# Performance work log

Measured on AMD Instinct MI355X. Metric: run time of the kernel, lower is better.

## Reference

```python
import jax, jax.numpy as jnp
import numpy as np
import math

DIM = 1024
N_HEADS = 16
HEAD_DIM = DIM // N_HEADS
FFN_HIDDEN = 4096
EPS = 1e-6


def setup_inputs() -> dict:
    key = jax.random.key(0)
    ks = jax.random.split(key, 10)
    s = 1.0 / math.sqrt(DIM)
    sh = 1.0 / math.sqrt(FFN_HIDDEN)
    return {
        "x": jax.random.normal(ks[0], (2, 2048, DIM), dtype=jnp.float32),
        # attention weights stored as [in, out] (y = x @ W)
        "wq": jax.random.normal(ks[1], (DIM, DIM), dtype=jnp.float32) * s,
        "wk": jax.random.normal(ks[2], (DIM, DIM), dtype=jnp.float32) * s,
        "wv": jax.random.normal(ks[3], (DIM, DIM), dtype=jnp.float32) * s,
        "wo": jax.random.normal(ks[4], (DIM, DIM), dtype=jnp.float32) * s,
        "w_gate": jax.random.normal(ks[5], (DIM, FFN_HIDDEN), dtype=jnp.float32) * s,
        "w_up": jax.random.normal(ks[6], (DIM, FFN_HIDDEN), dtype=jnp.float32) * s,
        "w_down": jax.random.normal(ks[7], (FFN_HIDDEN, DIM), dtype=jnp.float32) * sh,
        "attn_norm_w": jnp.ones((DIM,), dtype=jnp.float32),
        "ffn_norm_w": jnp.ones((DIM,), dtype=jnp.float32),
    }


def rmsnorm(x, w):
    xf = x.astype(jnp.float32)
    rms = jax.lax.rsqrt(jnp.mean(xf * xf, axis=-1, keepdims=True) + EPS)
    return (xf * rms).astype(x.dtype) * w


def attention(x, wq, wk, wv, wo):
    B, T, C = x.shape
    q = (x @ wq).reshape(B, T, N_HEADS, HEAD_DIM)
    k = (x @ wk).reshape(B, T, N_HEADS, HEAD_DIM)
    v = (x @ wv).reshape(B, T, N_HEADS, HEAD_DIM)
    scores = jnp.einsum("bqhd,bkhd->bhqk", q, k) / math.sqrt(HEAD_DIM)
    causal = jnp.tril(jnp.ones((T, T), dtype=bool))  # True = keep
    scores = jnp.where(causal, scores, -jnp.inf)
    attn = jax.nn.softmax(scores, axis=-1)
    out = jnp.einsum("bhqk,bkhd->bqhd", attn, v).reshape(B, T, C)
    return out @ wo


def swiglu(x, w_gate, w_up, w_down):
    return (jax.nn.silu(x @ w_gate) * (x @ w_up)) @ w_down


def reference(x, wq, wk, wv, wo, w_gate, w_up, w_down, attn_norm_w, ffn_norm_w):
    x = x + attention(rmsnorm(x, attn_norm_w), wq, wk, wv, wo)
    x = x + swiglu(rmsnorm(x, ffn_norm_w), w_gate, w_up, w_down)
    return x
```

## Files before the change

kernel.cpp:

```cpp
#include <hip/hip_runtime.h>
#include <hip/hip_bf16.h>
#include <stdint.h>
#include <math.h>

#define DIM   1024
#define TSEQ  2048
#define BATCH 2
#define NH    16
#define HD    64
#define FFN   4096
#define ROWS  (BATCH*TSEQ)
#define QKVN  (3*DIM)

typedef __attribute__((ext_vector_type(8))) short s16x8;
typedef __attribute__((ext_vector_type(4))) float f32x4;

__device__ __forceinline__ unsigned short f2bf(float f) {
  union { float f; unsigned u; } v; v.f = f;
  unsigned r = v.u + 0x7fffu + ((v.u >> 16) & 1u);
  return (unsigned short)(r >> 16);
}
__device__ __forceinline__ float bf2f(unsigned short h) {
  union { unsigned u; float f; } v; v.u = ((unsigned)h) << 16; return v.f;
}
__device__ __forceinline__ unsigned pack_bf2(float lo, float hi) {
  union { float f; unsigned u; } a, c; a.f = lo; c.f = hi;
  return (c.u & 0xffff0000u) | (a.u >> 16);
}

__device__ __forceinline__ void gld16(const void* g, void* l) {
  __builtin_amdgcn_global_load_lds((const __attribute__((address_space(1))) void*)g,
                                   (__attribute__((address_space(3))) void*)l, 16, 0, 0);
}

__device__ __forceinline__ int xcd_swz_flat() {
  const int nx = gridDim.x, ny = gridDim.y;
  const int nwg = nx * ny * gridDim.z;
  const int flat = blockIdx.x + nx * (blockIdx.y + ny * blockIdx.z);
  return (flat & 7) * (nwg >> 3) + (flat >> 3);
}

__global__ void wtrans_k(const float* __restrict__ w, unsigned short* __restrict__ wt,
                         int K, int N, int mode)
{
  __shared__ unsigned short t[64][65];
  const int n0 = blockIdx.x * 64, k0 = blockIdx.y * 64;
  const int tid = threadIdx.x;
  #pragma unroll
  for (int i = 0; i < 16; ++i) {
    const int r = i*4 + (tid >> 6), c = tid & 63;
    t[r][c] = f2bf(w[(size_t)(k0 + r) * N + n0 + c]);
  }
  __syncthreads();
  #pragma unroll
  for (int i = 0; i < 16; ++i) {
    const int r = i*4 + (tid >> 6), c = tid & 63;
    const int n = n0 + r;
    int dr = n;
    if (mode == 1) dr = ((n >> 4) << 5) + (n & 15);
    if (mode == 2) dr = ((n >> 4) << 5) + 16 + (n & 15);
    wt[(size_t)dr * K + k0 + c] = t[c][r];
  }
}

__global__ void wtrans_qkv_k(const float* __restrict__ wq, const float* __restrict__ wk,
                             const float* __restrict__ wv, unsigned short* __restrict__ wt)
{
  __shared__ unsigned short t[64][65];
  const int n0 = blockIdx.x * 64, k0 = blockIdx.y * 64, z = blockIdx.z;
  const float* w = (z == 0) ? wq : (z == 1) ? wk : wv;
  unsigned short* dst = wt + (size_t)z * DIM * DIM;
  const int tid = threadIdx.x;
  #pragma unroll
  for (int i = 0; i < 16; ++i) {
    const int r = i*4 + (tid >> 6), c = tid & 63;
    t[r][c] = f2bf(w[(size_t)(k0 + r) * DIM + n0 + c]);
  }
  __syncthreads();
  #pragma unroll
  for (int i = 0; i < 16; ++i) {
    const int r = i*4 + (tid >> 6), c = tid & 63;
    dst[(size_t)(n0 + r) * DIM + k0 + c] = t[c][r];
  }
}

__global__ void vtrans_k(const unsigned short* __restrict__ qkv, unsigned short* __restrict__ vt)
{
  __shared__ unsigned short t[64][65];
  const int tt0 = blockIdx.x * 64;
  const int bh = blockIdx.y, b = bh >> 4, h = bh & 15;
  const int tid = threadIdx.x;
  const unsigned short* src = qkv + (size_t)(b*TSEQ + tt0) * QKVN + 2*DIM + h*HD;
  #pragma unroll
  for (int i = 0; i < 16; ++i) {
    const int r = i*4 + (tid >> 6), c = tid & 63;
    t[r][c] = src[(size_t)r * QKVN + c];
  }
  __syncthreads();
  unsigned short* dst = vt + (size_t)bh * HD * TSEQ + tt0;
  #pragma unroll
  for (int i = 0; i < 16; ++i) {
    const int d = i*4 + (tid >> 6), c = tid & 63;
    dst[(size_t)d * TSEQ + c] = t[c][d];
  }
}

__global__ void rmsnorm_k(const float* __restrict__ x, const float* __restrict__ w,
                          unsigned short* __restrict__ o)
{
  const int row = blockIdx.x, tid = threadIdx.x;
  const float4 v = ((const float4*)(x + (size_t)row * DIM))[tid];
  float ss = v.x*v.x + v.y*v.y + v.z*v.z + v.w*v.w;
  #pragma unroll
  for (int off = 32; off >= 1; off >>= 1) ss += __shfl_xor(ss, off);
  __shared__ float sred[4];
  if ((tid & 63) == 0) sred[tid >> 6] = ss;
  __syncthreads();
  const float tot = sred[0] + sred[1] + sred[2] + sred[3];
  const float r = rsqrtf(tot * (1.0f/DIM) + 1e-6f);
  const float4 wv = ((const float4*)w)[tid];
  ushort4 ov;
  ov.x = f2bf(v.x*r*wv.x); ov.y = f2bf(v.y*r*wv.y);
  ov.z = f2bf(v.z*r*wv.z); ov.w = f2bf(v.w*r*wv.w);
  ((ushort4*)(o + (size_t)row * DIM))[tid] = ov;
}

__global__ void rmsnorm3_k(const float* __restrict__ x, const unsigned short* __restrict__ p0,
                           const unsigned short* __restrict__ p1, const float* __restrict__ w,
                           float* __restrict__ x1, unsigned short* __restrict__ o)
{
  const int row = blockIdx.x, tid = threadIdx.x;
  const size_t base = (size_t)row * DIM;
  const float4 a = ((const float4*)(x + base))[tid];
  const ushort4 b = ((const ushort4*)(p0 + base))[tid];
  const ushort4 c = ((const ushort4*)(p1 + base))[tid];
  float4 v;
  v.x = a.x + bf2f(b.x) + bf2f(c.x); v.y = a.y + bf2f(b.y) + bf2f(c.y);
  v.z = a.z + bf2f(b.z) + bf2f(c.z); v.w = a.w + bf2f(b.w) + bf2f(c.w);
  ((float4*)(x1 + base))[tid] = v;
  float ss = v.x*v.x + v.y*v.y + v.z*v.z + v.w*v.w;
  #pragma unroll
  for (int off = 32; off >= 1; off >>= 1) ss += __shfl_xor(ss, off);
  __shared__ float sred[4];
  if ((tid & 63) == 0) sred[tid >> 6] = ss;
  __syncthreads();
  const float tot = sred[0] + sred[1] + sred[2] + sred[3];
  const float r = rsqrtf(tot * (1.0f/DIM) + 1e-6f);
  const float4 wv = ((const float4*)w)[tid];
  ushort4 ov;
  ov.x = f2bf(v.x*r*wv.x); ov.y = f2bf(v.y*r*wv.y);
  ov.z = f2bf(v.z*r*wv.z); ov.w = f2bf(v.w*r*wv.w);
  ((ushort4*)(o + base))[tid] = ov;
}

__global__ void resadd5_k(const float* __restrict__ x1,
                          const unsigned short* __restrict__ q0, const unsigned short* __restrict__ q1,
                          const unsigned short* __restrict__ q2, const unsigned short* __restrict__ q3,
                          float* __restrict__ o)
{
  const size_t i = (size_t)blockIdx.x * 256 + threadIdx.x;
  const float4 a = ((const float4*)x1)[i];
  const ushort4 b = ((const ushort4*)q0)[i];
  const ushort4 c = ((const ushort4*)q1)[i];
  const ushort4 d = ((const ushort4*)q2)[i];
  const ushort4 e = ((const ushort4*)q3)[i];
  float4 v;
  v.x = a.x + bf2f(b.x) + bf2f(c.x) + bf2f(d.x) + bf2f(e.x);
  v.y = a.y + bf2f(b.y) + bf2f(c.y) + bf2f(d.y) + bf2f(e.y);
  v.z = a.z + bf2f(b.z) + bf2f(c.z) + bf2f(d.z) + bf2f(e.z);
  v.w = a.w + bf2f(b.w) + bf2f(c.w) + bf2f(d.w) + bf2f(e.w);
  ((float4*)o)[i] = v;
}

template<int NS>
__global__ void gemm128sp(const unsigned short* __restrict__ A, int lda,
                          const unsigned short* __restrict__ BT, int ldb,
                          unsigned short* __restrict__ P, int ldc, int Ksp)
{
  __shared__ __align__(16) unsigned short lA[128*64];
  __shared__ __align__(16) unsigned short lB[128*64];
  const int nx = gridDim.x, ny = gridDim.y;
  const int w = xcd_swz_flat();
  const int bx = w % nx, by = (w / nx) % ny, bz = w / (nx * ny);
  const int tid = threadIdx.x;
  const int lane = tid & 63;
  const int wid = tid >> 6;
  const int m0 = by * 128, n0 = bx * 128;
  const int Koff = bz * Ksp;
  P += (size_t)bz * ((size_t)ny * 128) * ldc;
  const int wr = (wid >> 1) * 64, wc = (wid & 1) * 64;
  const int lrow = lane & 15, lk8 = (lane >> 4) * 8;

  f32x4 acc[4][4] = {};

  for (int k0 = Koff; k0 < Koff + Ksp; k0 += 64) {
    #pragma unroll
    for (int c = 0; c < 4; ++c) {
      const int boff = c*4096 + tid*16;
      const int row = boff >> 7, colb = boff & 127;
      gld16((const char*)A + ((size_t)(m0+row)*lda + k0)*2 + colb, (char*)lA + boff);
    }
    #pragma unroll
    for (int c = 0; c < 4; ++c) {
      const int boff = c*4096 + tid*16;
      const int row = boff >> 7, colb = boff & 127;
      gld16((const char*)BT + ((size_t)(n0+row)*ldb + k0)*2 + colb, (char*)lB + boff);
    }
    __syncthreads();
    #pragma unroll
    for (int kk = 0; kk < 64; kk += 32) {
      s16x8 af[4], bf[4];
      #pragma unroll
      for (int i = 0; i < 4; ++i) af[i] = *(const s16x8*)&lA[(wr + i*16 + lrow)*64 + kk + lk8];
      #pragma unroll
      for (int j = 0; j < 4; ++j) bf[j] = *(const s16x8*)&lB[(wc + j*16 + lrow)*64 + kk + lk8];
      #pragma unroll
      for (int i = 0; i < 4; ++i)
        #pragma unroll
        for (int j = 0; j < 4; ++j)
          acc[i][j] = __builtin_amdgcn_mfma_f32_16x16x32_bf16(af[i], bf[j], acc[i][j], 0, 0, 0);
    }
    __syncthreads();
  }
  const int er = (lane >> 4) * 4, ec = lane & 15;
  #pragma unroll
  for (int i = 0; i < 4; ++i)
    #pragma unroll
    for (int j = 0; j < 4; ++j) {
      const int gr = m0 + wr + i*16 + er;
      const int gc = n0 + wc + j*16 + ec;
      #pragma unroll
      for (int e = 0; e < 4; ++e)
        P[(size_t)(gr + e) * ldc + gc] = f2bf(acc[i][j][e]);
    }
}

template<int EPI>
__global__ __launch_bounds__(512) void gemm256(const unsigned short* __restrict__ A, int lda,
                                               const unsigned short* __restrict__ BT, int ldb,
                                               void* __restrict__ Cout, int ldc, int K,
                                               int CX, int CY)
{
  __shared__ __align__(16) unsigned short lA[2][256*64];
  __shared__ __align__(16) unsigned short lB[2][256*64];
  const int nx = gridDim.x, ny = gridDim.y;
  const int flat = blockIdx.x + nx * blockIdx.y;
  const int xcd = flat & 7, k = flat >> 3;
  const int RX = nx / CX, RY = ny / CY;
  const int cx = xcd % CX, cy = xcd / CX;
  const int bx = cx * RX + k % RX;
  const int by = cy * RY + k / RX;
  const int tid = threadIdx.x, lane = tid & 63, wid = tid >> 6;
  const int lrow = lane & 15, g = lane >> 4;
  const int wm = wid >> 2, wn = wid & 3;
  const int m0 = by * 256, n0 = bx * 256;

  const int r0 = tid >> 3;
  const int eB = ((r0 >> 5) << 6) | (r0 & 31);
  const int lc0 = ((tid & 7) * 16) ^ ((r0 & 7) << 4);
  const char* pA = (const char*)A + ((size_t)(m0 + r0) * lda) * 2 + lc0;
  const char* pB = (const char*)BT + ((size_t)(n0 + eB) * ldb) * 2 + lc0;
  char* dA = (char*)&lA[0][0] + tid * 16;
  char* dB = (char*)&lB[0][0] + eB * 128 + (tid & 7) * 16;
  const size_t a64 = (size_t)64 * lda * 2;
  const size_t b32 = (size_t)32 * ldb * 2;

#define STG_GA0(t) do { const char* s_ = pA + (size_t)(t) * 128; \
    char* d_ = dA + (((t) & 1) * 32768); \
    gld16(s_, d_); gld16(s_ + 2*a64, d_ + 16384); } while (0)
#define STG_GA1(t) do { const char* s_ = pA + (size_t)(t) * 128 + a64; \
    char* d_ = dA + (((t) & 1) * 32768) + 8192; \
    gld16(s_, d_); gld16(s_ + 2*a64, d_ + 16384); } while (0)
#define STG_GB0(t) do { const char* s_ = pB + (size_t)(t) * 128; \
    char* d_ = dB + (((t) & 1) * 32768); \
    gld16(s_, d_); gld16(s_ + 4*b32, d_ + 16384); } while (0)
#define STG_GB1(t) do { const char* s_ = pB + (size_t)(t) * 128 + b32; \
    char* d_ = dB + (((t) & 1) * 32768) + 4096; \
    gld16(s_, d_); gld16(s_ + 4*b32, d_ + 16384); } while (0)

  const int swz = (lrow & 7) << 4;
  const int c0 = (g * 16) ^ swz;
  const int c1 = c0 ^ 64;
  const char* rdA = (const char*)&lA[0][0] + (wm * 128 + lrow) * 128;
  const char* rdB = (const char*)&lB[0][0] + (wn * 64 + lrow) * 128;

  f32x4 acc[8][4] = {};
  s16x8 a0[4][2], a1[4][2], b0[2][2], b1[2][2];

#define MFMA_Q(rh, ch, AF, BF) do { \
    _Pragma("unroll") \
    for (int i_ = 0; i_ < 4; ++i_) { \
      _Pragma("unroll") \
      for (int j_ = 0; j_ < 2; ++j_) { \
        acc[(rh)*4+i_][(ch)*2+j_] = __builtin_amdgcn_mfma_f32_16x16x32_bf16(AF[i_][0], BF[j_][0], acc[(rh)*4+i_][(ch)*2+j_], 0,0,0); \
        acc[(rh)*4+i_][(ch)*2+j_] = __builtin_amdgcn_mfma_f32_16x16x32_bf16(AF[i_][1], BF[j_][1], acc[(rh)*4+i_][(ch)*2+j_], 0,0,0); \
      } } } while (0)

  const int NT = K >> 6;

  STG_GA0(0); STG_GB0(0); STG_GB1(0); STG_GA1(0);
  asm volatile("s_waitcnt vmcnt(4)" ::: "memory");
  __builtin_amdgcn_s_barrier();

  for (int t = 0; t < NT; ++t) {
    const char* bufA = rdA + (t & 1) * 32768;
    const char* bufB = rdB + (t & 1) * 32768;
    const bool more = (t + 1 < NT);
    #pragma unroll
    for (int i = 0; i < 4; ++i) {
      a0[i][0] = *(const s16x8*)(bufA + i*2048 + c0);
      a0[i][1] = *(const s16x8*)(bufA + i*2048 + c1);
    }
    #pragma unroll
    for (int j = 0; j < 2; ++j) {
      b0[j][0] = *(const s16x8*)(bufB + j*2048 + c0);
      b0[j][1] = *(const s16x8*)(bufB + j*2048 + c1);
    }
    if (more) { STG_GA0(t + 1); STG_GB0(t + 1); }
    __builtin_amdgcn_s_barrier();
    asm volatile("s_waitcnt lgkmcnt(0)" ::: "memory");
    __builtin_amdgcn_sched_barrier(0);
    __builtin_amdgcn_s_setprio(1);
    MFMA_Q(0, 0, a0, b0);
    __builtin_amdgcn_s_setprio(0);
    if (more) { asm volatile("s_waitcnt vmcnt(6)" ::: "memory"); }
    else      { asm volatile("s_waitcnt vmcnt(2)" ::: "memory"); }
    __builtin_amdgcn_s_barrier();
    #pragma unroll
    for (int j = 0; j < 2; ++j) {
      b1[j][0] = *(const s16x8*)(bufB + 4096 + j*2048 + c0);
      b1[j][1] = *(const s16x8*)(bufB + 4096 + j*2048 + c1);
    }
    if (more) STG_GB1(t + 1);
    __builtin_amdgcn_s_barrier();
    asm volatile("s_waitcnt lgkmcnt(0)" ::: "memory");
    __builtin_amdgcn_sched_barrier(0);
    __builtin_amdgcn_s_setprio(1);
    MFMA_Q(0, 1, a0, b1);
    __builtin_amdgcn_s_setprio(0);
    if (more) { asm volatile("s_waitcnt vmcnt(6)" ::: "memory"); }
    else      { asm volatile("s_waitcnt vmcnt(0)" ::: "memory"); }
    __builtin_amdgcn_s_barrier();
    #pragma unroll
    for (int i = 0; i < 4; ++i) {
      a1[i][0] = *(const s16x8*)(bufA + 8192 + i*2048 + c0);
      a1[i][1] = *(const s16x8*)(bufA + 8192 + i*2048 + c1);
    }
    if (more) STG_GA1(t + 1);
    __builtin_amdgcn_s_barrier();
    asm volatile("s_waitcnt lgkmcnt(0)" ::: "memory");
    __builtin_amdgcn_sched_barrier(0);
    __builtin_amdgcn_s_setprio(1);
    MFMA_Q(1, 1, a1, b1);
    __builtin_amdgcn_s_setprio(0);
    __builtin_amdgcn_s_barrier();
    __builtin_amdgcn_s_setprio(1);
    MFMA_Q(1, 0, a1, b0);
    __builtin_amdgcn_s_setprio(0);
    if (more) { asm volatile("s_waitcnt vmcnt(4)" ::: "memory"); }
    __builtin_amdgcn_s_barrier();
  }

  const int er = g * 4, ec = lane & 15;
  if (EPI == 0) {
    unsigned short* C = (unsigned short*)Cout;
    #pragma unroll
    for (int i = 0; i < 8; ++i)
      #pragma unroll
      for (int j = 0; j < 4; ++j) {
        const int gr = m0 + wm*128 + i*16 + er;
        const int gc = n0 + wn*64 + j*16 + ec;
        #pragma unroll
        for (int e = 0; e < 4; ++e)
          C[(size_t)(gr + e) * ldc + gc] = f2bf(acc[i][j][e]);
      }
  } else {
    unsigned short* C = (unsigned short*)Cout;
    #pragma unroll
    for (int i = 0; i < 8; ++i)
      #pragma unroll
      for (int tp = 0; tp < 2; ++tp) {
        const int gr = m0 + wm*128 + i*16 + er;
        const int hc = (n0 >> 1) + wn*32 + tp*16 + ec;
        #pragma unroll
        for (int e = 0; e < 4; ++e) {
          const float gv = acc[i][2*tp][e];
          const float uv = acc[i][2*tp + 1][e];
          const float hv = gv / (1.f + __expf(-gv)) * uv;
          C[(size_t)(gr + e) * ldc + hc] = f2bf(hv);
        }
      }
  }
#undef STG_GA0
#undef STG_GA1
#undef STG_GB0
#undef STG_GB1
#undef MFMA_Q
}

__global__ __launch_bounds__(512) void attn_fwd(const unsigned short* __restrict__ qkv,
                                                const unsigned short* __restrict__ vt,
                                                unsigned short* __restrict__ outp)
{
  __shared__ __align__(16) unsigned short lK[2][64*64];
  __shared__ __align__(16) unsigned short lV[2][64*64];
  const int nx = gridDim.x;
  const int wsz = xcd_swz_flat();
  const int qblk = wsz % nx;
  const int bh = wsz / nx, b = bh >> 4, h = bh & 15;
  const int tid = threadIdx.x, wid = tid >> 6, lane = tid & 63;
  const int lq = lane & 15, g = lane >> 4;

  const int qrow = qblk*128 + wid*16;
  const int myq = qrow + lq;

  const size_t qbase = ((size_t)(b*TSEQ + myq)) * QKVN + h*HD;
  const s16x8 qf0 = *(const s16x8*)&qkv[qbase + g*8];
  const s16x8 qf1 = *(const s16x8*)&qkv[qbase + 32 + g*8];

  const int boff = tid * 16;
  const int loff = boff ^ (((boff >> 7) & 7) << 4);
  const int srow = loff >> 7;
  const int scolb = loff & 127;
  const char* ksrc0 = (const char*)qkv +
      (((size_t)(b*TSEQ + srow)) * QKVN + DIM + h*HD) * 2 + scolb;
  const char* vsrc0 = (const char*)vt +
      (((size_t)bh*HD + srow) * TSEQ) * 2 + scolb;

  float mrun = -INFINITY, lrun = 0.f;
  f32x4 of[4] = {};

  const int nkt = 2*qblk + 2;

  gld16(ksrc0, (char*)lK[0] + boff);
  gld16(vsrc0, (char*)lV[0] + boff);
  int cur = 0;

  for (int kt = 0; kt < nkt; ++kt) {
    __syncthreads();
    if (kt + 1 < nkt) {
      gld16(ksrc0 + (size_t)(kt+1)*64*(QKVN*2), (char*)lK[cur^1] + boff);
      gld16(vsrc0 + (size_t)(kt+1)*128,         (char*)lV[cur^1] + boff);
    }
    if (kt*64 <= qrow + 15) {
      const unsigned short* Kb = lK[cur];
      const unsigned short* Vb = lV[cur];
      f32x4 sacc[4] = {};
      #pragma unroll
      for (int s = 0; s < 4; ++s) {
        const int r = s*16 + lq;
        const int sw = (r & 7) << 4;
        const s16x8 kf0 = *(const s16x8*)((const char*)Kb + r*128 + ((g*16) ^ sw));
        const s16x8 kf1 = *(const s16x8*)((const char*)Kb + r*128 + ((64 + g*16) ^ sw));
        sacc[s] = __builtin_amdgcn_mfma_f32_16x16x32_bf16(kf0, qf0, sacc[s], 0,0,0);
        sacc[s] = __builtin_amdgcn_mfma_f32_16x16x32_bf16(kf1, qf1, sacc[s], 0,0,0);
      }
      float p[4][4];
      float mt = -INFINITY;
      #pragma unroll
      for (int s = 0; s < 4; ++s)
        #pragma unroll
        for (int e = 0; e < 4; ++e) {
          const int key = kt*64 + s*16 + 4*g + e;
          const float v = (key <= myq) ? sacc[s][e]*0.125f : -INFINITY;
          p[s][e] = v;
          mt = fmaxf(mt, v);
        }
      mt = fmaxf(mt, __shfl_xor(mt, 16));
      mt = fmaxf(mt, __shfl_xor(mt, 32));
      const float mnew = fmaxf(mrun, mt);
      const float scale = __expf(mrun - mnew);
      float ssum = 0.f;
      #pragma unroll
      for (int s = 0; s < 4; ++s)
        #pragma unroll
        for (int e = 0; e < 4; ++e) {
          p[s][e] = __expf(p[s][e] - mnew);
          ssum += p[s][e];
        }
      ssum += __shfl_xor(ssum, 16);
      ssum += __shfl_xor(ssum, 32);
      lrun = lrun * scale + ssum;
      mrun = mnew;
      #pragma unroll
      for (int d0b = 0; d0b < 4; ++d0b) of[d0b] = of[d0b] * scale;
      #pragma unroll
      for (int hh = 0; hh < 2; ++hh) {
        unsigned w[4];
        #pragma unroll
        for (int j = 0; j < 4; ++j) w[j] = pack_bf2(p[2*hh][j], p[2*hh+1][j]);
        s16x8 bp;
        #pragma unroll
        for (int e = 0; e < 8; ++e) {
          const int srcg = 2*(g & 1) + (e >> 2);
          const unsigned ww = (unsigned)__shfl((int)w[e & 3], lq | (srcg << 4));
          bp[e] = (short)((g >= 2) ? (ww >> 16) : (ww & 0xffffu));
        }
        #pragma unroll
        for (int d0b = 0; d0b < 4; ++d0b) {
          const int r = d0b*16 + lq;
          const int sw = (r & 7) << 4;
          const s16x8 vf = *(const s16x8*)((const char*)Vb + r*128 + ((hh*64 + g*16) ^ sw));
          of[d0b] = __builtin_amdgcn_mfma_f32_16x16x32_bf16(vf, bp, of[d0b], 0,0,0);
        }
      }
    }
    cur ^= 1;
  }
  const float inv = 1.f / lrun;
  const size_t obase = ((size_t)(b*TSEQ + myq)) * DIM + h*HD;
  #pragma unroll
  for (int d0b = 0; d0b < 4; ++d0b) {
    ushort4 o;
    o.x = f2bf(of[d0b][0] * inv);
    o.y = f2bf(of[d0b][1] * inv);
    o.z = f2bf(of[d0b][2] * inv);
    o.w = f2bf(of[d0b][3] * inv);
    *(ushort4*)&outp[obase + d0b*16 + 4*g] = o;
  }
}

extern "C" void kernel_launch(void* const* d_in, const int* in_sizes, int n_in,
                              void* d_out, int out_size, void* d_ws, size_t ws_size,
                              hipStream_t stream)
{
  const float* x   = (const float*)d_in[0];
  const float* wq  = (const float*)d_in[1];
  const float* wk  = (const float*)d_in[2];
  const float* wv  = (const float*)d_in[3];
  const float* wo  = (const float*)d_in[4];
  const float* wg  = (const float*)d_in[5];
  const float* wu  = (const float*)d_in[6];
  const float* wd  = (const float*)d_in[7];
  const float* anw = (const float*)d_in[8];
  const float* fnw = (const float*)d_in[9];
  float* outp = (float*)d_out;

  const size_t MB = 1024*1024;
  const size_t RD = (size_t)ROWS * DIM;
  char* ws = (char*)d_ws;
  float*          x1    = (float*)         (ws + 0);
  unsigned short* wdT   = (unsigned short*)(ws + 16*MB);
  unsigned short* wguT  = (unsigned short*)(ws + 24*MB);
  unsigned short* wqkvT = (unsigned short*)(ws + 40*MB);
  unsigned short* woT   = (unsigned short*)(ws + 46*MB);
  unsigned short* xn    = (unsigned short*)(ws + 48*MB);
  unsigned short* qkv   = (unsigned short*)(ws + 56*MB);
  unsigned short* vtb   = (unsigned short*)(ws + 80*MB);
  unsigned short* aout  = (unsigned short*)(ws + 88*MB);
  unsigned short* pwo   = (unsigned short*)(ws + 56*MB);
  unsigned short* hbuf  = (unsigned short*)(ws + 56*MB);
  unsigned short* pdn   = (unsigned short*)(ws + 24*MB);

  const dim3 blk(256);

  wtrans_qkv_k<<<dim3(16,16,3), blk, 0, stream>>>(wq, wk, wv, wqkvT);
  wtrans_k<<<dim3(16,16), blk, 0, stream>>>(wo, woT, DIM, DIM, 0);
  wtrans_k<<<dim3(64,16), blk, 0, stream>>>(wg, wguT, DIM, FFN, 1);
  wtrans_k<<<dim3(64,16), blk, 0, stream>>>(wu, wguT, DIM, FFN, 2);
  wtrans_k<<<dim3(16,64), blk, 0, stream>>>(wd, wdT, FFN, DIM, 0);

  rmsnorm_k<<<ROWS, blk, 0, stream>>>(x, anw, xn);
  gemm256<0><<<dim3(QKVN/256, ROWS/256), dim3(512), 0, stream>>>(xn, DIM, wqkvT, DIM, qkv, QKVN, DIM, 4, 2);
  vtrans_k<<<dim3(TSEQ/64, BATCH*NH), blk, 0, stream>>>(qkv, vtb);
  attn_fwd<<<dim3(TSEQ/128, BATCH*NH), dim3(512), 0, stream>>>(qkv, vtb, aout);
  gemm128sp<2><<<dim3(DIM/128, ROWS/128, 2), blk, 0, stream>>>(aout, DIM, woT, DIM, pwo, DIM, DIM/2);
  rmsnorm3_k<<<ROWS, blk, 0, stream>>>(x, pwo, pwo + RD, fnw, x1, xn);

  gemm256<2><<<dim3(2*FFN/256, ROWS/256), dim3(512), 0, stream>>>(xn, DIM, wguT, DIM, hbuf, FFN, DIM, 4, 2);
  gemm128sp<4><<<dim3(DIM/128, ROWS/128, 4), blk, 0, stream>>>(hbuf, FFN, wdT, FFN, pdn, DIM, FFN/4);
  resadd5_k<<<dim3(ROWS*DIM/1024), blk, 0, stream>>>(x1, pdn, pdn + RD, pdn + 2*RD, pdn + 3*RD, outp);
}
```

Before: 299.9 us.

## Single-buffer LDS in gemm256, staging next tile after compute

Replaces the double-buffered LDS ping-pong in the 256x256 GEMM with a single buffer per operand, halving shared memory from 128KB to 64KB. The next K-tile is now loaded only after all MFMAs and a barrier, and the kernel waits for vmcnt(0) at the top of each iteration. The intent is to allow higher occupancy (two blocks per CU) and simpler synchronization, at the cost of no longer overlapping global loads with MFMA work inside a block.

```diff
diff --git a/kernel.cpp b/kernel.cpp
--- a/kernel.cpp
+++ b/kernel.cpp
@@ -241,15 +241,15 @@
                                                void* __restrict__ Cout, int ldc, int K,
                                                int CX, int CY)
 {
-  __shared__ __align__(16) unsigned short lA[2][256*64];
-  __shared__ __align__(16) unsigned short lB[2][256*64];
+  __shared__ __align__(16) unsigned short lA[256*64];
+  __shared__ __align__(16) unsigned short lB[256*64];
   const int nx = gridDim.x, ny = gridDim.y;
   const int flat = blockIdx.x + nx * blockIdx.y;
-  const int xcd = flat & 7, k = flat >> 3;
+  const int xcd = flat & 7, kk_ = flat >> 3;
   const int RX = nx / CX, RY = ny / CY;
   const int cx = xcd % CX, cy = xcd / CX;
-  const int bx = cx * RX + k % RX;
-  const int by = cy * RY + k / RX;
+  const int bx = cx * RX + kk_ % RX;
+  const int by = cy * RY + kk_ / RX;
   const int tid = threadIdx.x, lane = tid & 63, wid = tid >> 6;
   const int lrow = lane & 15, g = lane >> 4;
   const int wm = wid >> 2, wn = wid & 3;
@@ -260,29 +260,25 @@
   const int lc0 = ((tid & 7) * 16) ^ ((r0 & 7) << 4);
   const char* pA = (const char*)A + ((size_t)(m0 + r0) * lda) * 2 + lc0;
   const char* pB = (const char*)BT + ((size_t)(n0 + eB) * ldb) * 2 + lc0;
-  char* dA = (char*)&lA[0][0] + tid * 16;
-  char* dB = (char*)&lB[0][0] + eB * 128 + (tid & 7) * 16;
+  char* dA = (char*)&lA[0] + tid * 16;
+  char* dB = (char*)&lB[0] + eB * 128 + (tid & 7) * 16;
   const size_t a64 = (size_t)64 * lda * 2;
   const size_t b32 = (size_t)32 * ldb * 2;
 
-#define STG_GA0(t) do { const char* s_ = pA + (size_t)(t) * 128; \
-    char* d_ = dA + (((t) & 1) * 32768); \
-    gld16(s_, d_); gld16(s_ + 2*a64, d_ + 16384); } while (0)
-#define STG_GA1(t) do { const char* s_ = pA + (size_t)(t) * 128 + a64; \
-    char* d_ = dA + (((t) & 1) * 32768) + 8192; \
-    gld16(s_, d_); gld16(s_ + 2*a64, d_ + 16384); } while (0)
-#define STG_GB0(t) do { const char* s_ = pB + (size_t)(t) * 128; \
-    char* d_ = dB + (((t) & 1) * 32768); \
-    gld16(s_, d_); gld16(s_ + 4*b32, d_ + 16384); } while (0)
-#define STG_GB1(t) do { const char* s_ = pB + (size_t)(t) * 128 + b32; \
-    char* d_ = dB + (((t) & 1) * 32768) + 4096; \
-    gld16(s_, d_); gld16(s_ + 4*b32, d_ + 16384); } while (0)
+#define STAGE(t) do { \
+    const char* sa_ = pA + (size_t)(t) * 128; \
+    gld16(sa_, dA);                 gld16(sa_ + 2*a64, dA + 16384); \
+    gld16(sa_ + a64, dA + 8192);    gld16(sa_ + 3*a64, dA + 24576); \
+    const char* sb_ = pB + (size_t)(t) * 128; \
+    gld16(sb_, dB);                 gld16(sb_ + 4*b32, dB + 16384); \
+    gld16(sb_ + b32, dB + 4096);    gld16(sb_ + 5*b32, dB + 20480); \
+  } while (0)
 
   const int swz = (lrow & 7) << 4;
   const int c0 = (g * 16) ^ swz;
   const int c1 = c0 ^ 64;
-  const char* rdA = (const char*)&lA[0][0] + (wm * 128 + lrow) * 128;
-  const char* rdB = (const char*)&lB[0][0] + (wn * 64 + lrow) * 128;
+  const char* rdA = (const char*)&lA[0] + (wm * 128 + lrow) * 128;
+  const char* rdB = (const char*)&lB[0] + (wn * 64 + lrow) * 128;
 
   f32x4 acc[8][4] = {};
   s16x8 a0[4][2], a1[4][2], b0[2][2], b1[2][2];
@@ -296,69 +292,49 @@
         acc[(rh)*4+i_][(ch)*2+j_] = __builtin_amdgcn_mfma_f32_16x16x32_bf16(AF[i_][1], BF[j_][1], acc[(rh)*4+i_][(ch)*2+j_], 0,0,0); \
       } } } while (0)
 
+#define VMCNT(n) asm volatile("s_waitcnt vmcnt(" #n ")" ::: "memory")
+#define LGKM(n)  do { asm volatile("s_waitcnt lgkmcnt(" #n ")" ::: "memory"); \
+                      __builtin_amdgcn_sched_barrier(0); } while (0)
+#define BARRIER() do { __builtin_amdgcn_s_barrier(); \
+                       __builtin_amdgcn_sched_barrier(0); } while (0)
+
+#define RD_A0() do { _Pragma("unroll") for (int i_ = 0; i_ < 4; ++i_) { \
+    a0[i_][0] = *(const s16x8*)(rdA + i_*2048 + c0); \
+    a0[i_][1] = *(const s16x8*)(rdA + i_*2048 + c1); } } while (0)
+#define RD_A1() do { _Pragma("unroll") for (int i_ = 0; i_ < 4; ++i_) { \
+    a1[i_][0] = *(const s16x8*)(rdA + 8192 + i_*2048 + c0); \
+    a1[i_][1] = *(const s16x8*)(rdA + 8192 + i_*2048 + c1); } } while (0)
+#define RD_B0() do { _Pragma("unroll") for (int j_ = 0; j_ < 2; ++j_) { \
+    b0[j_][0] = *(const s16x8*)(rdB + j_*2048 + c0); \
+    b0[j_][1] = *(const s16x8*)(rdB + j_*2048 + c1); } } while (0)
+#define RD_B1() do { _Pragma("unroll") for (int j_ = 0; j_ < 2; ++j_) { \
+    b1[j_][0] = *(const s16x8*)(rdB + 4096 + j_*2048 + c0); \
+    b1[j_][1] = *(const s16x8*)(rdB + 4096 + j_*2048 + c1); } } while (0)
+
   const int NT = K >> 6;
 
-  STG_GA0(0); STG_GB0(0); STG_GB1(0); STG_GA1(0);
-  asm volatile("s_waitcnt vmcnt(4)" ::: "memory");
-  __builtin_amdgcn_s_barrier();
+  STAGE(0);
 
   for (int t = 0; t < NT; ++t) {
-    const char* bufA = rdA + (t & 1) * 32768;
-    const char* bufB = rdB + (t & 1) * 32768;
-    const bool more = (t + 1 < NT);
-    #pragma unroll
-    for (int i = 0; i < 4; ++i) {
-      a0[i][0] = *(const s16x8*)(bufA + i*2048 + c0);
-      a0[i][1] = *(const s16x8*)(bufA + i*2048 + c1);
-    }
-    #pragma unroll
-    for (int j = 0; j < 2; ++j) {
-      b0[j][0] = *(const s16x8*)(bufB + j*2048 + c0);
-      b0[j][1] = *(const s16x8*)(bufB + j*2048 + c1);
-    }
-    if (more) { STG_GA0(t + 1); STG_GB0(t + 1); }
-    __builtin_amdgcn_s_barrier();
-    asm volatile("s_waitcnt lgkmcnt(0)" ::: "memory");
-    __builtin_amdgcn_sched_barrier(0);
+    VMCNT(0);
+    BARRIER();
+    RD_A0(); RD_B0(); RD_B1();
+    LGKM(4);
     __builtin_amdgcn_s_setprio(1);
     MFMA_Q(0, 0, a0, b0);
     __builtin_amdgcn_s_setprio(0);
-    if (more) { asm volatile("s_waitcnt vmcnt(6)" ::: "memory"); }
-    else      { asm volatile("s_waitcnt vmcnt(2)" ::: "memory"); }
-    __builtin_amdgcn_s_barrier();
-    #pragma unroll
-    for (int j = 0; j < 2; ++j) {
-      b1[j][0] = *(const s16x8*)(bufB + 4096 + j*2048 + c0);
-      b1[j][1] = *(const s16x8*)(bufB + 4096 + j*2048 + c1);
-    }
-    if (more) STG_GB1(t + 1);
-    __builtin_amdgcn_s_barrier();
-    asm volatile("s_waitcnt lgkmcnt(0)" ::: "memory");
-    __builtin_amdgcn_sched_barrier(0);
+    LGKM(0);
     __builtin_amdgcn_s_setprio(1);
     MFMA_Q(0, 1, a0, b1);
     __builtin_amdgcn_s_setprio(0);
-    if (more) { asm volatile("s_waitcnt vmcnt(6)" ::: "memory"); }
-    else      { asm volatile("s_waitcnt vmcnt(0)" ::: "memory"); }
-    __builtin_amdgcn_s_barrier();
-    #pragma unroll
-    for (int i = 0; i < 4; ++i) {
-      a1[i][0] = *(const s16x8*)(bufA + 8192 + i*2048 + c0);
-      a1[i][1] = *(const s16x8*)(bufA + 8192 + i*2048 + c1);
-    }
-    if (more) STG_GA1(t + 1);
-    __builtin_amdgcn_s_barrier();
-    asm volatile("s_waitcnt lgkmcnt(0)" ::: "memory");
-    __builtin_amdgcn_sched_barrier(0);
+    RD_A1();
+    LGKM(0);
     __builtin_amdgcn_s_setprio(1);
+    MFMA_Q(1, 0, a1, b0);
     MFMA_Q(1, 1, a1, b1);
     __builtin_amdgcn_s_setprio(0);
-    __builtin_amdgcn_s_barrier();
-    __builtin_amdgcn_s_setprio(1);
-    MFMA_Q(1, 0, a1, b0);
-    __builtin_amdgcn_s_setprio(0);
-    if (more) { asm volatile("s_waitcnt vmcnt(4)" ::: "memory"); }
-    __builtin_amdgcn_s_barrier();
+    BARRIER();
+    if (t + 1 < NT) STAGE(t + 1);
   }
 
   const int er = g * 4, ec = lane & 15;
@@ -391,11 +367,15 @@
         }
       }
   }
-#undef STG_GA0
-#undef STG_GA1
-#undef STG_GB0
-#undef STG_GB1
+#undef STAGE
 #undef MFMA_Q
+#undef VMCNT
+#undef LGKM
+#undef BARRIER
+#undef RD_A0
+#undef RD_A1
+#undef RD_B0
+#undef RD_B1
 }
 
 __global__ __launch_bounds__(512) void attn_fwd(const unsigned short* __restrict__ qkv,
```

Result: slower. 312.0 us (+4.0%).
